# Performance work log

Hardware: AMD Instinct MI355X
Metric: run time of the kernel (lower is better)

Reference implementation:

```python
import jax, jax.numpy as jnp
import numpy as np

B, S, DIM, H = 2, 2048, 1024, 16
HD = DIM // H  # 64


def setup_inputs() -> dict:
    key = jax.random.key(0)
    ks = jax.random.split(key, 7)
    sc = 1.0 / np.sqrt(DIM)
    gammas = jnp.asarray(1.0 - 2.0 ** (-5.0 - np.arange(H)), jnp.float32)  # RetNet per-head decay
    return {
        "q": jax.random.normal(ks[0], (B, S, DIM), jnp.float32),
        "k": jax.random.normal(ks[1], (B, S, DIM), jnp.float32),
        "v": jax.random.normal(ks[2], (B, S, DIM), jnp.float32),
        "W_in": jax.random.normal(ks[3], (DIM, DIM), jnp.float32) * sc,
        "b_in": jnp.zeros((DIM,), jnp.float32),
        "W_gate": jax.random.normal(ks[4], (DIM, DIM), jnp.float32) * sc,
        "b_gate": jnp.zeros((DIM,), jnp.float32),
        "W_out": jax.random.normal(ks[5], (DIM, DIM), jnp.float32) * sc,
        "b_out": jnp.zeros((DIM,), jnp.float32),
        "gammas": gammas,
    }


def _mamba(x, W_in, b_in, W_gate, b_gate, W_out, b_out):
    # Gated linear recurrence: h_t = a_t * h_{t-1} + u_t  (selective-scan style)
    u = x @ W_in + b_in          # [B,S,D]
    a = jax.nn.sigmoid(x @ W_gate + b_gate)  # [B,S,D] data-dependent decay gate

    def combine(c1, c2):
        a1, u1 = c1
        a2, u2 = c2
        return (a1 * a2, a2 * u1 + u2)

    _, h = jax.lax.associative_scan(combine, (a, u), axis=1)  # parallel scan over S
    return h @ W_out + b_out  # residual=False, dropout=0.0


def _retention(q, k, v, gammas):
    # Per-head decay-masked attention: out = ((Q K^T / sqrt(hd)) * D) V,
    # D[h,n,m] = gamma_h^(n-m) for n>=m else 0 (causal decay kernel).
    def split(x):
        return x.reshape(B, S, H, HD).transpose(0, 2, 1, 3)  # [B,H,S,HD]

    qh, kh, vh = split(q), split(k), split(v)
    idx = jnp.arange(S)
    diff = idx[:, None] - idx[None, :]                        # [S,S]
    expnt = jnp.maximum(diff, 0).astype(jnp.float32)
    D = jnp.where(diff >= 0, gammas[:, None, None] ** expnt, 0.0)  # [H,S,S]
    scores = jnp.einsum("bhnd,bhmd->bhnm", qh, kh) / np.sqrt(HD)
    out = jnp.einsum("bhnm,bhmd->bhnd", scores * D[None], vh)
    return out.transpose(0, 2, 1, 3).reshape(B, S, DIM)


def reference(q, k, v, W_in, b_in, W_gate, b_gate, W_out, b_out, gammas):
    q_proj = _mamba(q, W_in, b_in, W_gate, b_gate, W_out, b_out)
    return _retention(q_proj, k, v, gammas)
```

## Files before the change

### kernel.cpp

```cpp
#include <hip/hip_runtime.h>
#include <math.h>

#define B_  2
#define S_  2048
#define D_  1024
#define H_  16
#define HD_ 64
#define M_  (B_*S_)

typedef unsigned short ushort_t;
typedef unsigned int   uint_t;
typedef __attribute__((ext_vector_type(8))) short bf16x8;
typedef __attribute__((ext_vector_type(4))) float f32x4;

__device__ __forceinline__ ushort_t f2bf(float f) {
    uint_t u = __builtin_bit_cast(uint_t, f);
    u += 0x7FFFu + ((u >> 16) & 1u);
    return (ushort_t)(u >> 16);
}
__device__ __forceinline__ float bf2f(ushort_t h) {
    uint_t u = (uint_t)h << 16;
    return __builtin_bit_cast(float, u);
}
__device__ __forceinline__ uint_t pkt(float lo, float hi) {
    return __builtin_amdgcn_perm(__builtin_bit_cast(uint_t, hi),
                                 __builtin_bit_cast(uint_t, lo), 0x07060302u);
}
__device__ __forceinline__ void dma16(const ushort_t* g, ushort_t* l) {
    __builtin_amdgcn_global_load_lds(
        (const __attribute__((address_space(1))) uint_t*)g,
        (__attribute__((address_space(3))) uint_t*)l, 16, 0, 0);
}
__device__ __forceinline__ bf16x8 fragr(const ushort_t* base, int row, int chunk) {
    return *(const bf16x8*)&base[row * 64 + (((chunk ^ (row & 7)) << 3))];
}

__global__ __launch_bounds__(256)
void prep(const float* __restrict__ W0, const float* __restrict__ W1,
          const float* __restrict__ W2, ushort_t* __restrict__ T0,
          ushort_t* __restrict__ T1, ushort_t* __restrict__ T2,
          const float* __restrict__ q, ushort_t* __restrict__ q_bf,
          const float* __restrict__ K, const float* __restrict__ V,
          const float* __restrict__ gammas, ushort_t* __restrict__ Kb,
          ushort_t* __restrict__ VT, ushort_t* __restrict__ Gg) {
    __shared__ ushort_t sh[9216];
    const int bi = blockIdx.x;
    const int tid = threadIdx.x;

    if (bi < 3072) {
        float* T = (float*)sh;
        const int z = bi >> 10, rem = bi & 1023;
        const int kt = rem & 31, nt = rem >> 5;
        const float*  W  = (z == 0) ? W0 : (z == 1) ? W1 : W2;
        ushort_t*     WT = (z == 0) ? T0 : (z == 1) ? T1 : T2;
        const int rr = tid >> 3, cc = (tid & 7) * 4;
        float4 w4 = *(const float4*)(W + (size_t)(kt * 32 + rr) * D_ + nt * 32 + cc);
        T[rr * 36 + cc + 0] = w4.x; T[rr * 36 + cc + 1] = w4.y;
        T[rr * 36 + cc + 2] = w4.z; T[rr * 36 + cc + 3] = w4.w;
        __syncthreads();
        ushort_t o[4];
        #pragma unroll
        for (int j = 0; j < 4; ++j) o[j] = f2bf(T[(cc + j) * 36 + rr]);
        *(ushort4*)(WT + (size_t)(nt * 32 + rr) * D_ + kt * 32 + cc) =
            make_ushort4(o[0], o[1], o[2], o[3]);
        return;
    }
    if (bi < 7168) {
        const int i = ((bi - 3072) * 256 + tid) * 4;
        float4 x = *(const float4*)(q + i);
        *(ushort4*)(q_bf + i) = make_ushort4(f2bf(x.x), f2bf(x.y), f2bf(x.z), f2bf(x.w));
        return;
    }
    ushort_t* Tv = sh;
    ushort_t* Tk = sh + 4608;
    const int rem = bi - 7168;
    const int mt = rem & 31, h = (rem >> 5) & 15, b = rem >> 9;
    const int m0 = mt * 64;
    const int r = tid >> 2, c0 = (tid & 3) * 16;
    const float lg = log2f(gammas[h]);
    const float gm = exp2f(-(float)r * lg);
    {
        const float* src = K + ((size_t)(b * S_ + m0 + r)) * D_ + h * HD_ + c0;
        ushort_t kb[16];
        #pragma unroll
        for (int j4 = 0; j4 < 4; ++j4) {
            float4 x = *(const float4*)(src + j4 * 4);
            kb[j4 * 4 + 0] = f2bf(x.x); kb[j4 * 4 + 1] = f2bf(x.y);
            kb[j4 * 4 + 2] = f2bf(x.z); kb[j4 * 4 + 3] = f2bf(x.w);
        }
        ushort_t* dst = Kb + ((size_t)(b * S_ + m0 + r)) * D_ + h * HD_ + c0;
        *(uint4*)(dst + 0) = *(const uint4*)&kb[0];
        *(uint4*)(dst + 8) = *(const uint4*)&kb[8];
        #pragma unroll
        for (int j = 0; j < 16; ++j) Tk[(c0 + j) * 72 + r] = kb[j];
    }
    {
        const float* src = V + ((size_t)(b * S_ + m0 + r)) * D_ + h * HD_ + c0;
        #pragma unroll
        for (int j4 = 0; j4 < 4; ++j4) {
            float4 x = *(const float4*)(src + j4 * 4);
            Tv[(c0 + j4 * 4 + 0) * 72 + r] = f2bf(x.x * gm);
            Tv[(c0 + j4 * 4 + 1) * 72 + r] = f2bf(x.y * gm);
            Tv[(c0 + j4 * 4 + 2) * 72 + r] = f2bf(x.z * gm);
            Tv[(c0 + j4 * 4 + 3) * 72 + r] = f2bf(x.w * gm);
        }
    }
    __syncthreads();
    {
        ushort_t* dst = VT + ((size_t)((b * H_ + h) * HD_ + r)) * S_ + m0 + c0;
        *(uint4*)(dst + 0) = *(const uint4*)&Tv[r * 72 + c0 + 0];
        *(uint4*)(dst + 8) = *(const uint4*)&Tv[r * 72 + c0 + 8];
    }
    const int w = tid >> 6, lane = tid & 63, quad = lane >> 4, l15 = lane & 15;
    bf16x8 af0 = *(const bf16x8*)&Tv[(w * 16 + l15) * 72 + quad * 8];
    bf16x8 af1 = *(const bf16x8*)&Tv[(w * 16 + l15) * 72 + 32 + quad * 8];
    ushort_t* gout = Gg + ((size_t)((b * H_ + h) * 32 + mt)) * 4096;
    #pragma unroll
    for (int kt2 = 0; kt2 < 4; ++kt2) {
        bf16x8 bf0 = *(const bf16x8*)&Tk[(kt2 * 16 + l15) * 72 + quad * 8];
        bf16x8 bf1 = *(const bf16x8*)&Tk[(kt2 * 16 + l15) * 72 + 32 + quad * 8];
        f32x4 g = {};
        g = __builtin_amdgcn_mfma_f32_16x16x32_bf16(af0, bf0, g, 0, 0, 0);
        g = __builtin_amdgcn_mfma_f32_16x16x32_bf16(af1, bf1, g, 0, 0, 0);
        #pragma unroll
        for (int reg = 0; reg < 4; ++reg)
            gout[(w * 16 + quad * 4 + reg) * 64 + kt2 * 16 + l15] = f2bf(g[reg]);
    }
}

__global__ __launch_bounds__(256)
void state_scan(const ushort_t* __restrict__ Gg, const float* __restrict__ gammas,
                ushort_t* __restrict__ Sb) {
    const int sl = blockIdx.x, h = blockIdx.y, b = blockIdx.z;
    const float g64 = exp2f(64.0f * log2f(gammas[h]));
    const int r = threadIdx.x >> 4;
    const int cb = (threadIdx.x & 15) * 4;
    const size_t base = ((size_t)((b * H_ + h) * 32)) * 4096 + (sl * 16 + r) * 64 + cb;
    float4 S = make_float4(0.f, 0.f, 0.f, 0.f);
    for (int c = 0; c < 32; ++c) {
        ushort4 g4 = *(const ushort4*)(Gg + base + (size_t)c * 4096);
        ushort4 sb;
        sb.x = f2bf(S.x); sb.y = f2bf(S.y); sb.z = f2bf(S.z); sb.w = f2bf(S.w);
        *(ushort4*)(Sb + base + (size_t)c * 4096) = sb;
        S.x = g64 * (S.x + bf2f(g4.x)); S.y = g64 * (S.y + bf2f(g4.y));
        S.z = g64 * (S.z + bf2f(g4.z)); S.w = g64 * (S.w + bf2f(g4.w));
    }
}

__global__ __launch_bounds__(256)
void gemm_dual_scan(const ushort_t* __restrict__ A, const ushort_t* __restrict__ BTi,
                    const ushort_t* __restrict__ BTg, const float* __restrict__ bi,
                    const float* __restrict__ bg, uint_t* __restrict__ PH,
                    float* __restrict__ cA, float* __restrict__ cU) {
    __shared__ ushort_t smem[32768];
    const int tid = threadIdx.x;
    const int n0 = blockIdx.x * 64, m0 = blockIdx.y * 128;
    const int w = tid >> 6, lane = tid & 63, quad = lane >> 4, l15 = lane & 15;
    const int wr = (w >> 1) * 64, wc = (w & 1) * 32;
    const int l8 = lane & 7, lr8 = lane >> 3;

    f32x4 acc_i[4][2] = {};
    f32x4 acc_g[4][2] = {};

    auto stage = [&](int k0, int bufo) {
        #pragma unroll
        for (int t = 0; t < 4; ++t) {
            const int row = w * 32 + t * 8 + lr8;
            const int gc = ((l8 ^ (row & 7)) << 3);
            dma16(A + (size_t)(m0 + row) * D_ + k0 + gc, &smem[bufo + row * 64 + l8 * 8]);
        }
        #pragma unroll
        for (int t = 0; t < 2; ++t) {
            const int row = w * 16 + t * 8 + lr8;
            const int gc = ((l8 ^ (row & 7)) << 3);
            dma16(BTi + (size_t)(n0 + row) * D_ + k0 + gc, &smem[bufo + 8192 + row * 64 + l8 * 8]);
            dma16(BTg + (size_t)(n0 + row) * D_ + k0 + gc, &smem[bufo + 12288 + row * 64 + l8 * 8]);
        }
    };

    stage(0, 0);
    __syncthreads();
    for (int t = 0; t < 16; ++t) {
        const int bufo = (t & 1) * 16384;
        if (t < 15) stage((t + 1) * 64, 16384 - bufo);
        const ushort_t* As = smem + bufo;
        const ushort_t* Bi = smem + bufo + 8192;
        const ushort_t* Bg = smem + bufo + 12288;
        #pragma unroll
        for (int kk = 0; kk < 2; ++kk) {
            bf16x8 af[4], bfi[2], bfg[2];
            #pragma unroll
            for (int i = 0; i < 4; ++i)
                af[i] = fragr(As, wr + 16 * i + l15, kk * 4 + quad);
            #pragma unroll
            for (int j = 0; j < 2; ++j) {
                bfi[j] = fragr(Bi, wc + 16 * j + l15, kk * 4 + quad);
                bfg[j] = fragr(Bg, wc + 16 * j + l15, kk * 4 + quad);
            }
            #pragma unroll
            for (int i = 0; i < 4; ++i)
                #pragma unroll
                for (int j = 0; j < 2; ++j) {
                    acc_i[i][j] = __builtin_amdgcn_mfma_f32_16x16x32_bf16(
                        af[i], bfi[j], acc_i[i][j], 0, 0, 0);
                    acc_g[i][j] = __builtin_amdgcn_mfma_f32_16x16x32_bf16(
                        af[i], bfg[j], acc_g[i][j], 0, 0, 0);
                }
        }
        __syncthreads();
    }

    ushort_t* Us = smem;
    ushort_t* Gu = smem + 8192;
    #pragma unroll
    for (int j = 0; j < 2; ++j) {
        const int n = wc + 16 * j + l15;
        const float bbi = bi[n0 + n], bbg = bg[n0 + n];
        #pragma unroll
        for (int i = 0; i < 4; ++i) {
            #pragma unroll
            for (int r = 0; r < 4; ++r) {
                const int m = wr + 16 * i + quad * 4 + r;
                Us[m * 64 + n] = f2bf(acc_i[i][j][r] + bbi);
                float g = 1.0f / (1.0f + __expf(-(acc_g[i][j][r] + bbg)));
                Gu[m * 64 + n] = (ushort_t)__float2uint_rn(g * 65535.0f);
            }
        }
    }
    __syncthreads();

    const int nl = tid & 63, c = tid >> 6;
    const int gmb = m0 + c * 32;
    const size_t gbase = (size_t)gmb * D_ + n0 + nl;
    float Aa = 1.0f, hh = 0.0f;
    #pragma unroll 4
    for (int j = 0; j < 32; ++j) {
        const float g = (float)Gu[(c * 32 + j) * 64 + nl] * (1.0f / 65535.0f);
        const float u = bf2f(Us[(c * 32 + j) * 64 + nl]);
        Aa *= g;
        hh = fmaf(g, hh, u);
        PH[gbase + (size_t)j * D_] = pkt(Aa, hh);
    }
    const int bb = gmb >> 11;
    const int ch = (gmb & 2047) >> 5;
    const int ci = ((bb * 64 + ch) << 10) + n0 + nl;
    cA[ci] = Aa;
    cU[ci] = hh;
}

__global__ __launch_bounds__(64)
void scan_pass2(const float* __restrict__ cA, const float* __restrict__ cU,
                float* __restrict__ cIn) {
    const int t = blockIdx.x * 64 + threadIdx.x;
    const int d = t & 1023, b = t >> 10;
    float h = 0.0f;
    for (int c0 = 0; c0 < 64; c0 += 16) {
        float Av[16], Uv[16];
        #pragma unroll
        for (int j = 0; j < 16; ++j) {
            const int idx = ((b * 64 + c0 + j) << 10) + d;
            Av[j] = cA[idx]; Uv[j] = cU[idx];
        }
        #pragma unroll
        for (int j = 0; j < 16; ++j) {
            cIn[((b * 64 + c0 + j) << 10) + d] = h;
            h = fmaf(Av[j], h, Uv[j]);
        }
    }
}

__global__ __launch_bounds__(256)
void scan_fix(const uint_t* __restrict__ PH, const float* __restrict__ cIn,
              ushort_t* __restrict__ hout) {
    const int i = (blockIdx.x * 256 + threadIdx.x) * 4;
    const int m = i >> 10, d = i & 1023;
    const int b = m >> 11, ch = (m & 2047) >> 5;
    uint4 p = *(const uint4*)(PH + i);
    float4 ci = *(const float4*)(cIn + ((b * 64 + ch) << 10) + d);
    ushort4 o;
    o.x = f2bf(fmaf(ci.x, bf2f((ushort_t)(p.x & 0xFFFF)), bf2f((ushort_t)(p.x >> 16))));
    o.y = f2bf(fmaf(ci.y, bf2f((ushort_t)(p.y & 0xFFFF)), bf2f((ushort_t)(p.y >> 16))));
    o.z = f2bf(fmaf(ci.z, bf2f((ushort_t)(p.z & 0xFFFF)), bf2f((ushort_t)(p.z >> 16))));
    o.w = f2bf(fmaf(ci.w, bf2f((ushort_t)(p.w & 0xFFFF)), bf2f((ushort_t)(p.w >> 16))));
    *(ushort4*)(hout + i) = o;
}

__global__ __launch_bounds__(256)
void retention_fused(const ushort_t* __restrict__ Hb, const ushort_t* __restrict__ WTo,
                     const float* __restrict__ bo, const ushort_t* __restrict__ Kb,
                     const ushort_t* __restrict__ VT, const ushort_t* __restrict__ Sb,
                     const float* __restrict__ gammas, float* __restrict__ Out) {
    __shared__ ushort_t smem[28672];
    const int tid = threadIdx.x;
    const int nt = blockIdx.x, h = blockIdx.y, b = blockIdx.z;
    const int n0 = nt * 64;
    const float lg = log2f(gammas[h]);
    const int w = tid >> 6, lane = tid & 63, quad = lane >> 4, l15 = lane & 15;
    const int l8 = lane & 7, lr8 = lane >> 3;
    const int nl = w * 16 + l15;
    const size_t bS = (size_t)b * S_;
    const size_t vrow0 = (size_t)((b * H_ + h) * HD_);
    const size_t sbase = ((size_t)((b * H_ + h) * 32 + nt)) * 4096;

    #pragma unroll
    for (int t = 0; t < 2; ++t) {
        const int row = w * 16 + t * 8 + lr8;
        const int gc = ((l8 ^ (row & 7)) << 3);
        dma16(Kb + (bS + n0 + row) * D_ + h * HD_ + gc, &smem[16384 + row * 64 + l8 * 8]);
        dma16(VT + (vrow0 + row) * S_ + n0 + gc,        &smem[20480 + row * 64 + l8 * 8]);
        dma16(Sb + sbase + (size_t)row * 64 + gc,       &smem[24576 + row * 64 + l8 * 8]);
    }

    auto stage = [&](int k0, int bufo) {
        #pragma unroll
        for (int t = 0; t < 2; ++t) {
            const int row = w * 8 + t * 32 + lr8;
            const int gc = ((l8 ^ (row & 7)) << 3);
            dma16(Hb + (bS + n0 + row) * D_ + k0 + gc, &smem[bufo + row * 64 + l8 * 8]);
            dma16(WTo + ((size_t)(h * 64 + row)) * D_ + k0 + gc,
                  &smem[bufo + 4096 + row * 64 + l8 * 8]);
        }
    };
    stage(0, 0);
    __syncthreads();

    f32x4 acc[4] = {};
    for (int t = 0; t < 16; ++t) {
        const int bufo = (t & 1) * 8192;
        if (t < 15) stage((t + 1) * 64, 8192 - bufo);
        const ushort_t* As = smem + bufo;
        const ushort_t* Bs = smem + bufo + 4096;
        #pragma unroll
        for (int kk = 0; kk < 2; ++kk) {
            bf16x8 af = fragr(As, w * 16 + l15, kk * 4 + quad);
            #pragma unroll
            for (int ct = 0; ct < 4; ++ct) {
                bf16x8 bf = fragr(Bs, ct * 16 + l15, kk * 4 + quad);
                acc[ct] = __builtin_amdgcn_mfma_f32_16x16x32_bf16(af, bf, acc[ct], 0, 0, 0);
            }
        }
        __syncthreads();
    }

    ushort_t* Qs = smem;
    ushort_t* Ps = smem + 4096;
    #pragma unroll
    for (int ct = 0; ct < 4; ++ct) {
        const int n = ct * 16 + l15;
        const float bb = bo[h * 64 + n];
        #pragma unroll
        for (int r = 0; r < 4; ++r) {
            const int m = w * 16 + quad * 4 + r;
            Qs[m * 64 + (((n >> 3) ^ (m & 7)) << 3) + (n & 7)] =
                f2bf((acc[ct][r] + bb) * 0.125f);
        }
    }
    __syncthreads();

    bf16x8 qf0 = fragr(Qs, nl, quad);
    bf16x8 qf1 = fragr(Qs, nl, 4 + quad);
    const ushort_t* Ks = smem + 16384;
    const ushort_t* Vt = smem + 20480;
    const ushort_t* Ss = smem + 24576;

    f32x4 o[4] = {};
    #pragma unroll
    for (int ct = 0; ct < 4; ++ct) {
        bf16x8 sf0 = fragr(Ss, ct * 16 + l15, quad);
        bf16x8 sf1 = fragr(Ss, ct * 16 + l15, 4 + quad);
        o[ct] = __builtin_amdgcn_mfma_f32_16x16x32_bf16(sf0, qf0, o[ct], 0, 0, 0);
        o[ct] = __builtin_amdgcn_mfma_f32_16x16x32_bf16(sf1, qf1, o[ct], 0, 0, 0);
    }
    #pragma unroll
    for (int mt2 = 0; mt2 < 4; ++mt2) {
        bf16x8 kf0 = fragr(Ks, mt2 * 16 + l15, quad);
        bf16x8 kf1 = fragr(Ks, mt2 * 16 + l15, 4 + quad);
        f32x4 s = {};
        s = __builtin_amdgcn_mfma_f32_16x16x32_bf16(kf0, qf0, s, 0, 0, 0);
        s = __builtin_amdgcn_mfma_f32_16x16x32_bf16(kf1, qf1, s, 0, 0, 0);
        const int mbase = mt2 * 16 + quad * 4;
        #pragma unroll
        for (int r = 0; r < 4; ++r)
            if (nl < mbase + r) s[r] = 0.0f;
        uint2 pw; pw.x = pkt(s[0], s[1]); pw.y = pkt(s[2], s[3]);
        const int chunk = mbase >> 3;
        *(uint2*)&Ps[nl * 64 + ((chunk ^ (nl & 7)) << 3) + (mbase & 7)] = pw;
    }
    bf16x8 pf0 = fragr(Ps, nl, quad);
    bf16x8 pf1 = fragr(Ps, nl, 4 + quad);
    #pragma unroll
    for (int ct = 0; ct < 4; ++ct) {
        bf16x8 vf0 = fragr(Vt, ct * 16 + l15, quad);
        bf16x8 vf1 = fragr(Vt, ct * 16 + l15, 4 + quad);
        o[ct] = __builtin_amdgcn_mfma_f32_16x16x32_bf16(vf0, pf0, o[ct], 0, 0, 0);
        o[ct] = __builtin_amdgcn_mfma_f32_16x16x32_bf16(vf1, pf1, o[ct], 0, 0, 0);
    }

    const float esc = exp2f((float)nl * lg);
    const size_t ob = (bS + n0 + nl) * D_ + h * HD_;
    #pragma unroll
    for (int ct = 0; ct < 4; ++ct) {
        f32x4 t = o[ct] * esc;
        *(f32x4*)(Out + ob + ct * 16 + quad * 4) = t;
    }
}

extern "C" void kernel_launch(void* const* d_in, const int* in_sizes, int n_in,
                              void* d_out, int out_size, void* d_ws, size_t ws_size,
                              hipStream_t stream) {
    const float* q      = (const float*)d_in[0];
    const float* k      = (const float*)d_in[1];
    const float* v      = (const float*)d_in[2];
    const float* W_in   = (const float*)d_in[3];
    const float* b_in   = (const float*)d_in[4];
    const float* W_gate = (const float*)d_in[5];
    const float* b_gate = (const float*)d_in[6];
    const float* W_out  = (const float*)d_in[7];
    const float* b_out  = (const float*)d_in[8];
    const float* gammas = (const float*)d_in[9];
    float* out = (float*)d_out;

    char* ws = (char*)d_ws;
    const size_t MB = 1024 * 1024;
    ushort_t* q_bf    = (ushort_t*)(ws);
    ushort_t* k_bf    = (ushort_t*)(ws + 8 * MB);
    ushort_t* VT      = (ushort_t*)(ws + 16 * MB);
    ushort_t* WT_in   = (ushort_t*)(ws + 24 * MB);
    ushort_t* WT_gate = (ushort_t*)(ws + 26 * MB);
    ushort_t* WT_out  = (ushort_t*)(ws + 28 * MB);
    ushort_t* Sb      = (ushort_t*)(ws + 30 * MB);
    ushort_t* Gg      = (ushort_t*)(ws + 38 * MB);
    uint_t*   PH      = (uint_t*)(ws + 48 * MB);
    ushort_t* h_bf    = (ushort_t*)(ws + 64 * MB);
    float*    cA      = (float*)(ws + 72 * MB);
    float*    cU      = (float*)(ws + 72 * MB + 512 * 1024);
    float*    cIn     = (float*)(ws + 73 * MB);

    prep<<<8192, 256, 0, stream>>>(W_in, W_gate, W_out, WT_in, WT_gate, WT_out,
                                   q, q_bf, k, v, gammas, k_bf, VT, Gg);

    state_scan<<<dim3(4, H_, B_), 256, 0, stream>>>(Gg, gammas, Sb);

    gemm_dual_scan<<<dim3(D_ / 64, M_ / 128), 256, 0, stream>>>(
        q_bf, WT_in, WT_gate, b_in, b_gate, PH, cA, cU);

    scan_pass2<<<32, 64, 0, stream>>>(cA, cU, cIn);
    scan_fix<<<(M_ * D_) / 1024, 256, 0, stream>>>(PH, cIn, h_bf);

    retention_fused<<<dim3(S_ / 64, H_, B_), 256, 0, stream>>>(
        h_bf, WT_out, b_out, k_bf, VT, Sb, gammas, out);
}
```

Measured before the change: 190.6 us.

## Load GEMM fragments directly from global memory and merge small scan kernels

Both GEMM stages (the dual in/gate projection and the out-projection inside the retention kernel) drop their LDS double-buffered DMA staging and __syncthreads, loading MFMA fragments directly from global memory through L1/L2. The state_scan and scan_pass2 kernels are merged into one mid_scan launch that dispatches on block index, removing one kernel launch. Shared memory use falls, which may raise occupancy. The cost is that each wave now issues redundant, less coalesced global loads with no cross-wave reuse in LDS, which may leave the GEMMs bound by memory latency.

```diff
diff --git a/kernel.cpp b/kernel.cpp
--- a/kernel.cpp
+++ b/kernel.cpp
@@ -129,89 +129,53 @@
 }
 
 __global__ __launch_bounds__(256)
-void state_scan(const ushort_t* __restrict__ Gg, const float* __restrict__ gammas,
-                ushort_t* __restrict__ Sb) {
-    const int sl = blockIdx.x, h = blockIdx.y, b = blockIdx.z;
-    const float g64 = exp2f(64.0f * log2f(gammas[h]));
-    const int r = threadIdx.x >> 4;
-    const int cb = (threadIdx.x & 15) * 4;
-    const size_t base = ((size_t)((b * H_ + h) * 32)) * 4096 + (sl * 16 + r) * 64 + cb;
-    float4 S = make_float4(0.f, 0.f, 0.f, 0.f);
-    for (int c = 0; c < 32; ++c) {
-        ushort4 g4 = *(const ushort4*)(Gg + base + (size_t)c * 4096);
-        ushort4 sb;
-        sb.x = f2bf(S.x); sb.y = f2bf(S.y); sb.z = f2bf(S.z); sb.w = f2bf(S.w);
-        *(ushort4*)(Sb + base + (size_t)c * 4096) = sb;
-        S.x = g64 * (S.x + bf2f(g4.x)); S.y = g64 * (S.y + bf2f(g4.y));
-        S.z = g64 * (S.z + bf2f(g4.z)); S.w = g64 * (S.w + bf2f(g4.w));
-    }
-}
-
-__global__ __launch_bounds__(256)
 void gemm_dual_scan(const ushort_t* __restrict__ A, const ushort_t* __restrict__ BTi,
                     const ushort_t* __restrict__ BTg, const float* __restrict__ bi,
                     const float* __restrict__ bg, uint_t* __restrict__ PH,
                     float* __restrict__ cA, float* __restrict__ cU) {
-    __shared__ ushort_t smem[32768];
+    __shared__ ushort_t Us[8192];
+    __shared__ ushort_t Gu[8192];
     const int tid = threadIdx.x;
     const int n0 = blockIdx.x * 64, m0 = blockIdx.y * 128;
     const int w = tid >> 6, lane = tid & 63, quad = lane >> 4, l15 = lane & 15;
     const int wr = (w >> 1) * 64, wc = (w & 1) * 32;
-    const int l8 = lane & 7, lr8 = lane >> 3;
 
     f32x4 acc_i[4][2] = {};
     f32x4 acc_g[4][2] = {};
 
-    auto stage = [&](int k0, int bufo) {
-        #pragma unroll
-        for (int t = 0; t < 4; ++t) {
-            const int row = w * 32 + t * 8 + lr8;
-            const int gc = ((l8 ^ (row & 7)) << 3);
-            dma16(A + (size_t)(m0 + row) * D_ + k0 + gc, &smem[bufo + row * 64 + l8 * 8]);
-        }
-        #pragma unroll
-        for (int t = 0; t < 2; ++t) {
-            const int row = w * 16 + t * 8 + lr8;
-            const int gc = ((l8 ^ (row & 7)) << 3);
-            dma16(BTi + (size_t)(n0 + row) * D_ + k0 + gc, &smem[bufo + 8192 + row * 64 + l8 * 8]);
-            dma16(BTg + (size_t)(n0 + row) * D_ + k0 + gc, &smem[bufo + 12288 + row * 64 + l8 * 8]);
-        }
-    };
-
-    stage(0, 0);
-    __syncthreads();
-    for (int t = 0; t < 16; ++t) {
-        const int bufo = (t & 1) * 16384;
-        if (t < 15) stage((t + 1) * 64, 16384 - bufo);
-        const ushort_t* As = smem + bufo;
-        const ushort_t* Bi = smem + bufo + 8192;
-        const ushort_t* Bg = smem + bufo + 12288;
-        #pragma unroll
-        for (int kk = 0; kk < 2; ++kk) {
-            bf16x8 af[4], bfi[2], bfg[2];
-            #pragma unroll
-            for (int i = 0; i < 4; ++i)
-                af[i] = fragr(As, wr + 16 * i + l15, kk * 4 + quad);
+    const ushort_t* ap[4];
+    const ushort_t* bip[2];
+    const ushort_t* bgp[2];
+    #pragma unroll
+    for (int i = 0; i < 4; ++i)
+        ap[i] = A + (size_t)(m0 + wr + 16 * i + l15) * D_ + quad * 8;
+    #pragma unroll
+    for (int j = 0; j < 2; ++j) {
+        bip[j] = BTi + (size_t)(n0 + wc + 16 * j + l15) * D_ + quad * 8;
+        bgp[j] = BTg + (size_t)(n0 + wc + 16 * j + l15) * D_ + quad * 8;
+    }
+
+    #pragma unroll 2
+    for (int k0 = 0; k0 < D_; k0 += 32) {
+        bf16x8 af[4], bfi[2], bfg[2];
+        #pragma unroll
+        for (int i = 0; i < 4; ++i) af[i] = *(const bf16x8*)(ap[i] + k0);
+        #pragma unroll
+        for (int j = 0; j < 2; ++j) {
+            bfi[j] = *(const bf16x8*)(bip[j] + k0);
+            bfg[j] = *(const bf16x8*)(bgp[j] + k0);
+        }
+        #pragma unroll
+        for (int i = 0; i < 4; ++i)
             #pragma unroll
             for (int j = 0; j < 2; ++j) {
-                bfi[j] = fragr(Bi, wc + 16 * j + l15, kk * 4 + quad);
-                bfg[j] = fragr(Bg, wc + 16 * j + l15, kk * 4 + quad);
+                acc_i[i][j] = __builtin_amdgcn_mfma_f32_16x16x32_bf16(
+                    af[i], bfi[j], acc_i[i][j], 0, 0, 0);
+                acc_g[i][j] = __builtin_amdgcn_mfma_f32_16x16x32_bf16(
+                    af[i], bfg[j], acc_g[i][j], 0, 0, 0);
             }
-            #pragma unroll
-            for (int i = 0; i < 4; ++i)
-                #pragma unroll
-                for (int j = 0; j < 2; ++j) {
-                    acc_i[i][j] = __builtin_amdgcn_mfma_f32_16x16x32_bf16(
-                        af[i], bfi[j], acc_i[i][j], 0, 0, 0);
-                    acc_g[i][j] = __builtin_amdgcn_mfma_f32_16x16x32_bf16(
-                        af[i], bfg[j], acc_g[i][j], 0, 0, 0);
-                }
-        }
-        __syncthreads();
-    }
-
-    ushort_t* Us = smem;
-    ushort_t* Gu = smem + 8192;
+    }
+
     #pragma unroll
     for (int j = 0; j < 2; ++j) {
         const int n = wc + 16 * j + l15;
@@ -248,10 +212,29 @@
     cU[ci] = hh;
 }
 
-__global__ __launch_bounds__(64)
-void scan_pass2(const float* __restrict__ cA, const float* __restrict__ cU,
-                float* __restrict__ cIn) {
-    const int t = blockIdx.x * 64 + threadIdx.x;
+__global__ __launch_bounds__(256)
+void mid_scan(const ushort_t* __restrict__ Gg, const float* __restrict__ gammas,
+              ushort_t* __restrict__ Sb, const float* __restrict__ cA,
+              const float* __restrict__ cU, float* __restrict__ cIn) {
+    const int bi = blockIdx.x;
+    if (bi < 128) {
+        const int sl = bi & 3, h = (bi >> 2) & 15, b = bi >> 6;
+        const float g64 = exp2f(64.0f * log2f(gammas[h]));
+        const int r = threadIdx.x >> 4;
+        const int cb = (threadIdx.x & 15) * 4;
+        const size_t base = ((size_t)((b * H_ + h) * 32)) * 4096 + (sl * 16 + r) * 64 + cb;
+        float4 S = make_float4(0.f, 0.f, 0.f, 0.f);
+        for (int c = 0; c < 32; ++c) {
+            ushort4 g4 = *(const ushort4*)(Gg + base + (size_t)c * 4096);
+            ushort4 sb;
+            sb.x = f2bf(S.x); sb.y = f2bf(S.y); sb.z = f2bf(S.z); sb.w = f2bf(S.w);
+            *(ushort4*)(Sb + base + (size_t)c * 4096) = sb;
+            S.x = g64 * (S.x + bf2f(g4.x)); S.y = g64 * (S.y + bf2f(g4.y));
+            S.z = g64 * (S.z + bf2f(g4.z)); S.w = g64 * (S.w + bf2f(g4.w));
+        }
+        return;
+    }
+    const int t = (bi - 128) * 256 + threadIdx.x;
     const int d = t & 1023, b = t >> 10;
     float h = 0.0f;
     for (int c0 = 0; c0 < 64; c0 += 16) {
@@ -290,7 +273,12 @@
                      const float* __restrict__ bo, const ushort_t* __restrict__ Kb,
                      const ushort_t* __restrict__ VT, const ushort_t* __restrict__ Sb,
                      const float* __restrict__ gammas, float* __restrict__ Out) {
-    __shared__ ushort_t smem[28672];
+    __shared__ ushort_t smem[20480];
+    ushort_t* Qs = smem;
+    ushort_t* Ps = smem + 4096;
+    ushort_t* Ks = smem + 8192;
+    ushort_t* Vt = smem + 12288;
+    ushort_t* Ss = smem + 16384;
     const int tid = threadIdx.x;
     const int nt = blockIdx.x, h = blockIdx.y, b = blockIdx.z;
     const int n0 = nt * 64;
@@ -306,44 +294,28 @@
     for (int t = 0; t < 2; ++t) {
         const int row = w * 16 + t * 8 + lr8;
         const int gc = ((l8 ^ (row & 7)) << 3);
-        dma16(Kb + (bS + n0 + row) * D_ + h * HD_ + gc, &smem[16384 + row * 64 + l8 * 8]);
-        dma16(VT + (vrow0 + row) * S_ + n0 + gc,        &smem[20480 + row * 64 + l8 * 8]);
-        dma16(Sb + sbase + (size_t)row * 64 + gc,       &smem[24576 + row * 64 + l8 * 8]);
-    }
-
-    auto stage = [&](int k0, int bufo) {
-        #pragma unroll
-        for (int t = 0; t < 2; ++t) {
-            const int row = w * 8 + t * 32 + lr8;
-            const int gc = ((l8 ^ (row & 7)) << 3);
-            dma16(Hb + (bS + n0 + row) * D_ + k0 + gc, &smem[bufo + row * 64 + l8 * 8]);
-            dma16(WTo + ((size_t)(h * 64 + row)) * D_ + k0 + gc,
-                  &smem[bufo + 4096 + row * 64 + l8 * 8]);
-        }
-    };
-    stage(0, 0);
-    __syncthreads();
+        dma16(Kb + (bS + n0 + row) * D_ + h * HD_ + gc, &Ks[row * 64 + l8 * 8]);
+        dma16(VT + (vrow0 + row) * S_ + n0 + gc,        &Vt[row * 64 + l8 * 8]);
+        dma16(Sb + sbase + (size_t)row * 64 + gc,       &Ss[row * 64 + l8 * 8]);
+    }
+
+    const ushort_t* hp = Hb + (bS + n0 + w * 16 + l15) * D_ + quad * 8;
+    const ushort_t* wp[4];
+    #pragma unroll
+    for (int ct = 0; ct < 4; ++ct)
+        wp[ct] = WTo + ((size_t)(h * 64 + ct * 16 + l15)) * D_ + quad * 8;
 
     f32x4 acc[4] = {};
-    for (int t = 0; t < 16; ++t) {
-        const int bufo = (t & 1) * 8192;
-        if (t < 15) stage((t + 1) * 64, 8192 - bufo);
-        const ushort_t* As = smem + bufo;
-        const ushort_t* Bs = smem + bufo + 4096;
-        #pragma unroll
-        for (int kk = 0; kk < 2; ++kk) {
-            bf16x8 af = fragr(As, w * 16 + l15, kk * 4 + quad);
-            #pragma unroll
-            for (int ct = 0; ct < 4; ++ct) {
-                bf16x8 bf = fragr(Bs, ct * 16 + l15, kk * 4 + quad);
-                acc[ct] = __builtin_amdgcn_mfma_f32_16x16x32_bf16(af, bf, acc[ct], 0, 0, 0);
-            }
-        }
-        __syncthreads();
-    }
-
-    ushort_t* Qs = smem;
-    ushort_t* Ps = smem + 4096;
+    #pragma unroll 2
+    for (int k0 = 0; k0 < D_; k0 += 32) {
+        bf16x8 af = *(const bf16x8*)(hp + k0);
+        #pragma unroll
+        for (int ct = 0; ct < 4; ++ct) {
+            bf16x8 bf = *(const bf16x8*)(wp[ct] + k0);
+            acc[ct] = __builtin_amdgcn_mfma_f32_16x16x32_bf16(af, bf, acc[ct], 0, 0, 0);
+        }
+    }
+
     #pragma unroll
     for (int ct = 0; ct < 4; ++ct) {
         const int n = ct * 16 + l15;
@@ -359,9 +331,6 @@
 
     bf16x8 qf0 = fragr(Qs, nl, quad);
     bf16x8 qf1 = fragr(Qs, nl, 4 + quad);
-    const ushort_t* Ks = smem + 16384;
-    const ushort_t* Vt = smem + 20480;
-    const ushort_t* Ss = smem + 24576;
 
     f32x4 o[4] = {};
     #pragma unroll
@@ -439,12 +408,11 @@
     prep<<<8192, 256, 0, stream>>>(W_in, W_gate, W_out, WT_in, WT_gate, WT_out,
                                    q, q_bf, k, v, gammas, k_bf, VT, Gg);
 
-    state_scan<<<dim3(4, H_, B_), 256, 0, stream>>>(Gg, gammas, Sb);
-
     gemm_dual_scan<<<dim3(D_ / 64, M_ / 128), 256, 0, stream>>>(
         q_bf, WT_in, WT_gate, b_in, b_gate, PH, cA, cU);
 
-    scan_pass2<<<32, 64, 0, stream>>>(cA, cU, cIn);
+    mid_scan<<<136, 256, 0, stream>>>(Gg, gammas, Sb, cA, cU, cIn);
+
     scan_fix<<<(M_ * D_) / 1024, 256, 0, stream>>>(PH, cIn, h_bf);
 
     retention_fused<<<dim3(S_ / 64, H_, B_), 256, 0, stream>>>(
```

Measured after the change: 277.5 us. +45.6%, slower.

## Fuse scan fixup into retention A-tile load and merge small scan kernels

Applied to the files above, without the earlier changes.

Merges state_scan and scan_pass2 into one mid_scan launch whose blocks branch by index, removing one launch and letting the two small scans run concurrently. Removes the scan_fix kernel and the h_bf intermediate. retention_fused now reads packed (A,h) prefix data plus the chunk carry-ins and applies the fixup while staging the A tile into shared memory. This drops a full write and re-read of the hidden state. The cost is that the A operand now goes through synchronous register loads of 4-byte packed data instead of async DMA, and the fixup is recomputed by each of the 16 head blocks that share the same rows.

```diff
diff --git a/kernel.cpp b/kernel.cpp
--- a/kernel.cpp
+++ b/kernel.cpp
@@ -125,25 +125,6 @@
         #pragma unroll
         for (int reg = 0; reg < 4; ++reg)
             gout[(w * 16 + quad * 4 + reg) * 64 + kt2 * 16 + l15] = f2bf(g[reg]);
-    }
-}
-
-__global__ __launch_bounds__(256)
-void state_scan(const ushort_t* __restrict__ Gg, const float* __restrict__ gammas,
-                ushort_t* __restrict__ Sb) {
-    const int sl = blockIdx.x, h = blockIdx.y, b = blockIdx.z;
-    const float g64 = exp2f(64.0f * log2f(gammas[h]));
-    const int r = threadIdx.x >> 4;
-    const int cb = (threadIdx.x & 15) * 4;
-    const size_t base = ((size_t)((b * H_ + h) * 32)) * 4096 + (sl * 16 + r) * 64 + cb;
-    float4 S = make_float4(0.f, 0.f, 0.f, 0.f);
-    for (int c = 0; c < 32; ++c) {
-        ushort4 g4 = *(const ushort4*)(Gg + base + (size_t)c * 4096);
-        ushort4 sb;
-        sb.x = f2bf(S.x); sb.y = f2bf(S.y); sb.z = f2bf(S.z); sb.w = f2bf(S.w);
-        *(ushort4*)(Sb + base + (size_t)c * 4096) = sb;
-        S.x = g64 * (S.x + bf2f(g4.x)); S.y = g64 * (S.y + bf2f(g4.y));
-        S.z = g64 * (S.z + bf2f(g4.z)); S.w = g64 * (S.w + bf2f(g4.w));
     }
 }
 
@@ -248,10 +229,29 @@
     cU[ci] = hh;
 }
 
-__global__ __launch_bounds__(64)
-void scan_pass2(const float* __restrict__ cA, const float* __restrict__ cU,
-                float* __restrict__ cIn) {
-    const int t = blockIdx.x * 64 + threadIdx.x;
+__global__ __launch_bounds__(256)
+void mid_scan(const ushort_t* __restrict__ Gg, const float* __restrict__ gammas,
+              ushort_t* __restrict__ Sb, const float* __restrict__ cA,
+              const float* __restrict__ cU, float* __restrict__ cIn) {
+    const int bi = blockIdx.x;
+    if (bi < 128) {
+        const int sl = bi & 3, h = (bi >> 2) & 15, b = bi >> 6;
+        const float g64 = exp2f(64.0f * log2f(gammas[h]));
+        const int r = threadIdx.x >> 4;
+        const int cb = (threadIdx.x & 15) * 4;
+        const size_t base = ((size_t)((b * H_ + h) * 32)) * 4096 + (sl * 16 + r) * 64 + cb;
+        float4 S = make_float4(0.f, 0.f, 0.f, 0.f);
+        for (int c = 0; c < 32; ++c) {
+            ushort4 g4 = *(const ushort4*)(Gg + base + (size_t)c * 4096);
+            ushort4 sb;
+            sb.x = f2bf(S.x); sb.y = f2bf(S.y); sb.z = f2bf(S.z); sb.w = f2bf(S.w);
+            *(ushort4*)(Sb + base + (size_t)c * 4096) = sb;
+            S.x = g64 * (S.x + bf2f(g4.x)); S.y = g64 * (S.y + bf2f(g4.y));
+            S.z = g64 * (S.z + bf2f(g4.z)); S.w = g64 * (S.w + bf2f(g4.w));
+        }
+        return;
+    }
+    const int t = (bi - 128) * 256 + threadIdx.x;
     const int d = t & 1023, b = t >> 10;
     float h = 0.0f;
     for (int c0 = 0; c0 < 64; c0 += 16) {
@@ -270,26 +270,11 @@
 }
 
 __global__ __launch_bounds__(256)
-void scan_fix(const uint_t* __restrict__ PH, const float* __restrict__ cIn,
-              ushort_t* __restrict__ hout) {
-    const int i = (blockIdx.x * 256 + threadIdx.x) * 4;
-    const int m = i >> 10, d = i & 1023;
-    const int b = m >> 11, ch = (m & 2047) >> 5;
-    uint4 p = *(const uint4*)(PH + i);
-    float4 ci = *(const float4*)(cIn + ((b * 64 + ch) << 10) + d);
-    ushort4 o;
-    o.x = f2bf(fmaf(ci.x, bf2f((ushort_t)(p.x & 0xFFFF)), bf2f((ushort_t)(p.x >> 16))));
-    o.y = f2bf(fmaf(ci.y, bf2f((ushort_t)(p.y & 0xFFFF)), bf2f((ushort_t)(p.y >> 16))));
-    o.z = f2bf(fmaf(ci.z, bf2f((ushort_t)(p.z & 0xFFFF)), bf2f((ushort_t)(p.z >> 16))));
-    o.w = f2bf(fmaf(ci.w, bf2f((ushort_t)(p.w & 0xFFFF)), bf2f((ushort_t)(p.w >> 16))));
-    *(ushort4*)(hout + i) = o;
-}
-
-__global__ __launch_bounds__(256)
-void retention_fused(const ushort_t* __restrict__ Hb, const ushort_t* __restrict__ WTo,
-                     const float* __restrict__ bo, const ushort_t* __restrict__ Kb,
-                     const ushort_t* __restrict__ VT, const ushort_t* __restrict__ Sb,
-                     const float* __restrict__ gammas, float* __restrict__ Out) {
+void retention_fused(const uint_t* __restrict__ PH, const float* __restrict__ cIn,
+                     const ushort_t* __restrict__ WTo, const float* __restrict__ bo,
+                     const ushort_t* __restrict__ Kb, const ushort_t* __restrict__ VT,
+                     const ushort_t* __restrict__ Sb, const float* __restrict__ gammas,
+                     float* __restrict__ Out) {
     __shared__ ushort_t smem[28672];
     const int tid = threadIdx.x;
     const int nt = blockIdx.x, h = blockIdx.y, b = blockIdx.z;
@@ -311,23 +296,56 @@
         dma16(Sb + sbase + (size_t)row * 64 + gc,       &smem[24576 + row * 64 + l8 * 8]);
     }
 
-    auto stage = [&](int k0, int bufo) {
+    const int r = tid >> 2, cb = (tid & 3) * 2;
+    const int ch = ((n0 + r) & 2047) >> 5;
+    const size_t phrow = (bS + n0 + r) * D_;
+    const float* cip = cIn + (((size_t)b * 64 + ch) << 10);
+
+    auto stageA = [&](int k0, int bufo) {
+        ushort_t* Ab = smem + bufo;
+        #pragma unroll
+        for (int cc = 0; cc < 2; ++cc) {
+            const int c = cb + cc;
+            uint4 pa = *(const uint4*)(PH + phrow + k0 + c * 8);
+            uint4 pb = *(const uint4*)(PH + phrow + k0 + c * 8 + 4);
+            float4 ca = *(const float4*)(cip + k0 + c * 8);
+            float4 cb4 = *(const float4*)(cip + k0 + c * 8 + 4);
+            float h0 = fmaf(ca.x,  bf2f((ushort_t)(pa.x & 0xFFFF)), bf2f((ushort_t)(pa.x >> 16)));
+            float h1 = fmaf(ca.y,  bf2f((ushort_t)(pa.y & 0xFFFF)), bf2f((ushort_t)(pa.y >> 16)));
+            float h2 = fmaf(ca.z,  bf2f((ushort_t)(pa.z & 0xFFFF)), bf2f((ushort_t)(pa.z >> 16)));
+            float h3 = fmaf(ca.w,  bf2f((ushort_t)(pa.w & 0xFFFF)), bf2f((ushort_t)(pa.w >> 16)));
+            float h4 = fmaf(cb4.x, bf2f((ushort_t)(pb.x & 0xFFFF)), bf2f((ushort_t)(pb.x >> 16)));
+            float h5 = fmaf(cb4.y, bf2f((ushort_t)(pb.y & 0xFFFF)), bf2f((ushort_t)(pb.y >> 16)));
+            float h6 = fmaf(cb4.z, bf2f((ushort_t)(pb.z & 0xFFFF)), bf2f((ushort_t)(pb.z >> 16)));
+            float h7 = fmaf(cb4.w, bf2f((ushort_t)(pb.w & 0xFFFF)), bf2f((ushort_t)(pb.w >> 16)));
+            uint4 hw;
+            hw.x = pkt(h0, h1); hw.y = pkt(h2, h3);
+            hw.z = pkt(h4, h5); hw.w = pkt(h6, h7);
+            *(uint4*)&smem[bufo + r * 64 + ((c ^ (r & 7)) << 3)] = hw;
+        }
+        (void)Ab;
+    };
+    auto stageB = [&](int k0, int bufo) {
         #pragma unroll
         for (int t = 0; t < 2; ++t) {
             const int row = w * 8 + t * 32 + lr8;
             const int gc = ((l8 ^ (row & 7)) << 3);
-            dma16(Hb + (bS + n0 + row) * D_ + k0 + gc, &smem[bufo + row * 64 + l8 * 8]);
             dma16(WTo + ((size_t)(h * 64 + row)) * D_ + k0 + gc,
                   &smem[bufo + 4096 + row * 64 + l8 * 8]);
         }
     };
-    stage(0, 0);
+
+    stageB(0, 0);
+    stageA(0, 0);
     __syncthreads();
 
     f32x4 acc[4] = {};
     for (int t = 0; t < 16; ++t) {
         const int bufo = (t & 1) * 8192;
-        if (t < 15) stage((t + 1) * 64, 8192 - bufo);
+        if (t < 15) {
+            stageB((t + 1) * 64, 8192 - bufo);
+            stageA((t + 1) * 64, 8192 - bufo);
+        }
         const ushort_t* As = smem + bufo;
         const ushort_t* Bs = smem + bufo + 4096;
         #pragma unroll
@@ -349,10 +367,10 @@
         const int n = ct * 16 + l15;
         const float bb = bo[h * 64 + n];
         #pragma unroll
-        for (int r = 0; r < 4; ++r) {
-            const int m = w * 16 + quad * 4 + r;
+        for (int rr = 0; rr < 4; ++rr) {
+            const int m = w * 16 + quad * 4 + rr;
             Qs[m * 64 + (((n >> 3) ^ (m & 7)) << 3) + (n & 7)] =
-                f2bf((acc[ct][r] + bb) * 0.125f);
+                f2bf((acc[ct][rr] + bb) * 0.125f);
         }
     }
     __syncthreads();
@@ -380,8 +398,8 @@
         s = __builtin_amdgcn_mfma_f32_16x16x32_bf16(kf1, qf1, s, 0, 0, 0);
         const int mbase = mt2 * 16 + quad * 4;
         #pragma unroll
-        for (int r = 0; r < 4; ++r)
-            if (nl < mbase + r) s[r] = 0.0f;
+        for (int rr = 0; rr < 4; ++rr)
+            if (nl < mbase + rr) s[rr] = 0.0f;
         uint2 pw; pw.x = pkt(s[0], s[1]); pw.y = pkt(s[2], s[3]);
         const int chunk = mbase >> 3;
         *(uint2*)&Ps[nl * 64 + ((chunk ^ (nl & 7)) << 3) + (mbase & 7)] = pw;
@@ -431,7 +449,6 @@
     ushort_t* Sb      = (ushort_t*)(ws + 30 * MB);
     ushort_t* Gg      = (ushort_t*)(ws + 38 * MB);
     uint_t*   PH      = (uint_t*)(ws + 48 * MB);
-    ushort_t* h_bf    = (ushort_t*)(ws + 64 * MB);
     float*    cA      = (float*)(ws + 72 * MB);
     float*    cU      = (float*)(ws + 72 * MB + 512 * 1024);
     float*    cIn     = (float*)(ws + 73 * MB);
@@ -439,14 +456,11 @@
     prep<<<8192, 256, 0, stream>>>(W_in, W_gate, W_out, WT_in, WT_gate, WT_out,
                                    q, q_bf, k, v, gammas, k_bf, VT, Gg);
 
-    state_scan<<<dim3(4, H_, B_), 256, 0, stream>>>(Gg, gammas, Sb);
-
     gemm_dual_scan<<<dim3(D_ / 64, M_ / 128), 256, 0, stream>>>(
         q_bf, WT_in, WT_gate, b_in, b_gate, PH, cA, cU);
 
-    scan_pass2<<<32, 64, 0, stream>>>(cA, cU, cIn);
-    scan_fix<<<(M_ * D_) / 1024, 256, 0, stream>>>(PH, cIn, h_bf);
+    mid_scan<<<136, 256, 0, stream>>>(Gg, gammas, Sb, cA, cU, cIn);
 
     retention_fused<<<dim3(S_ / 64, H_, B_), 256, 0, stream>>>(
-        h_bf, WT_out, b_out, k_bf, VT, Sb, gammas, out);
-}
+        PH, cIn, WT_out, b_out, k_bf, VT, Sb, gammas, out);
+}
```

After: 201.7 us. +5.8%, slower.
